# Kernel optimization log

Measured on AMD Instinct MI355X. Metric: run time of the kernel, lower is better.

The kernel has to match this reference:

```python
import jax, jax.numpy as jnp
import numpy as np
from math import factorial

R_MAX = 3.5
BASIS = 20
NORM2MOM_SILU = 1.679177  # e3nn normalize2mom constant for silu

# ---------- Wigner 3j (e3nn convention: real basis, Frobenius norm 1) ----------

def _su2_cg(j1, m1, j2, m2, j3, m3):
    if m3 != m1 + m2:
        return 0.0
    vmin = int(max(-j1 + j2 + m3, -j1 + m1, 0))
    vmax = int(min(j2 + j3 + m1, j3 - j1 + j2, j3 + m3))
    f = lambda n: factorial(round(n))
    C = ((2 * j3 + 1) * f(j3 + j1 - j2) * f(j3 - j1 + j2) * f(j1 + j2 - j3)
         * f(j3 + m3) * f(j3 - m3)
         / (f(j1 + j2 + j3 + 1) * f(j1 - m1) * f(j1 + m1) * f(j2 - m2) * f(j2 + m2))) ** 0.5
    S = 0.0
    for v in range(vmin, vmax + 1):
        S += (-1.0) ** (v + j2 + m2) / f(v) * f(j2 + j3 + m1 - v) * f(j1 - m1 + v) \
             / f(j3 - j1 + j2 - v) / f(j3 + m3 - v) / f(v + j1 - j2 - m3)
    return C * S


def _real_basis(l):
    q = np.zeros((2 * l + 1, 2 * l + 1), dtype=np.complex128)
    for m in range(-l, 0):
        q[l + m, l + abs(m)] = 2 ** -0.5
        q[l + m, l - abs(m)] = -1j * 2 ** -0.5
    q[l, l] = 1.0
    for m in range(1, l + 1):
        q[l + m, l + abs(m)] = (-1) ** m * 2 ** -0.5
        q[l + m, l - abs(m)] = 1j * (-1) ** m * 2 ** -0.5
    return (-1j) ** l * q


def wigner_3j(l1, l2, l3):
    C = np.zeros((2 * l1 + 1, 2 * l2 + 1, 2 * l3 + 1))
    for m1 in range(-l1, l1 + 1):
        for m2 in range(-l2, l2 + 1):
            if abs(m1 + m2) <= l3:
                C[l1 + m1, l2 + m2, l3 + m1 + m2] = _su2_cg(l1, m1, l2, m2, l3, m1 + m2)
    Q1, Q2, Q3 = _real_basis(l1), _real_basis(l2), _real_basis(l3)
    Cr = np.einsum('ij,kl,mn,ikn->jlm', Q1, Q2, np.conj(Q3.T), C.astype(np.complex128))
    assert np.abs(Cr.imag).max() < 1e-4
    Cr = Cr.real
    return (Cr / np.linalg.norm(Cr)).astype(np.float32)

# tp2 paths: (l1 from middle, l2 from sh) -> 2e (even parity, triangle inequality)
TP2_PATHS = [(0, 2), (1, 1), (1, 3), (2, 0), (2, 2), (3, 1), (3, 3)]
W3J = {p: jnp.asarray(wigner_3j(p[0], p[1], 2)) for p in TP2_PATHS}
ALPHA2 = (5.0 / 35.0) ** 0.5  # component norm: sqrt(dim(2e) / fan_in), fan_in = 7 paths * mul 5

# ---------- spherical harmonics, lmax=3, component normalization (e3nn axis convention) ----------

def spherical_harmonics(v):  # v: [E,3] unit vectors -> [E,16]
    x, y, z = v[:, 0], v[:, 1], v[:, 2]
    x2, y2, z2 = x * x, y * y, z * z
    s3, s5, s15 = 3.0 ** 0.5, 5.0 ** 0.5, 15.0 ** 0.5
    s70_4, s105, s42_4 = 70.0 ** 0.5 / 4, 105.0 ** 0.5, 42.0 ** 0.5 / 4
    s7_2, s105_2 = 7.0 ** 0.5 / 2, 105.0 ** 0.5 / 2
    sh = [jnp.ones_like(x),
          s3 * x, s3 * y, s3 * z,
          s15 * x * z, s15 * x * y, s5 * (y2 - 0.5 * (x2 + z2)), s15 * y * z, 0.5 * s15 * (z2 - x2),
          s70_4 * x * (3 * z2 - x2), s105 * x * y * z, s42_4 * x * (5 * y2 - 1.0),
          s7_2 * y * (5 * y2 - 3.0), s42_4 * z * (5 * y2 - 1.0), s105_2 * y * (z2 - x2),
          s70_4 * z * (z2 - 3 * x2)]
    return jnp.stack(sh, axis=-1)


def soft_one_hot(d):  # smooth_finite basis with cutoff on [0, R_MAX]
    values = jnp.linspace(0.0, R_MAX, BASIS + 2)[1:-1]
    step = R_MAX / (BASIS + 1)
    diff = (d[:, None] - values) / step
    def u(t):
        ts = jnp.where(t > 0, t, 1.0)
        return jnp.where(t > 0, jnp.exp(-1.0 / ts), 0.0)
    return 1.14136 * np.e ** 2 * u(diff + 1.0) * u(1.0 - diff)


def setup_inputs() -> dict:
    key = jax.random.key(0)
    ks = jax.random.split(key, 7)
    N, E = 50000, 600000
    edge_from = jax.random.randint(ks[2], (E,), 0, N)
    # no self-loops (avoids zero-length edge vectors, as radius_graph would)
    edge_to = (edge_from + jax.random.randint(ks[3], (E,), 1, N)) % N
    return {
        'x': jax.random.normal(ks[0], (N, 1), jnp.float32),
        'pos': jax.random.normal(ks[1], (N, 3), jnp.float32),
        'edge_from': edge_from,
        'edge_to': edge_to,
        'W1': jax.random.normal(ks[4], (20, 30), jnp.float32),
        'W2': jax.random.normal(ks[5], (30, 20), jnp.float32),
        'tp2_w': jax.random.normal(ks[6], (7, 5), jnp.float32),
    }


def reference(x, pos, edge_from, edge_to, W1, W2, tp2_w):
    E = edge_from.shape[0]
    N = x.shape[0]
    num_neighbors = 6.0
    edge_vec = pos[edge_to] - pos[edge_from]                 # [E,3]
    dist = jnp.linalg.norm(edge_vec, axis=1)                 # [E]
    sh = spherical_harmonics(edge_vec / dist[:, None])       # [E,16]
    emb = soft_one_hot(dist)                                 # [E,20]
    # FullyConnectedNet([20,30,20], silu) with e3nn normalization
    h = NORM2MOM_SILU * jax.nn.silu(emb @ W1 / jnp.sqrt(20.0))
    tp_w = (h @ W2 / jnp.sqrt(30.0)).reshape(E, 4, 5)        # per-edge tp1 weights
    s = x[edge_to, 0]                                        # [E] gathered 0e scalars
    sh_blocks = [sh[:, 0:1], sh[:, 1:4], sh[:, 4:9], sh[:, 9:16]]
    # tp1: 0e x l -> l ; alpha * w3j(0,l,l) collapses to identity per l
    mid = jnp.concatenate([
        (s[:, None, None] * tp_w[:, l, :, None] * sh_blocks[l][:, None, :]).reshape(E, 5 * (2 * l + 1))
        for l in range(4)], axis=-1)                         # [E,80]
    node_mid = jax.ops.segment_sum(mid, edge_from, num_segments=N) / jnp.sqrt(num_neighbors)
    m = node_mid[edge_to]                                    # [E,80]
    offs = [0, 5, 20, 45, 80]
    mid_blocks = [m[:, offs[l]:offs[l + 1]].reshape(E, 5, 2 * l + 1) for l in range(4)]
    out_e = jnp.zeros((E, 5), dtype=x.dtype)
    for p, (l1, l2) in enumerate(TP2_PATHS):
        out_e = out_e + ALPHA2 * jnp.einsum('ijk,eui,ej,u->ek', W3J[(l1, l2)],
                                            mid_blocks[l1], sh_blocks[l2], tp2_w[p])
    node_out = jax.ops.segment_sum(out_e, edge_from, num_segments=N) / jnp.sqrt(num_neighbors)
    Co = jnp.argmax(jnp.bincount(edge_to, length=N))         # torch.mode -> most frequent target node
    return node_out[Co]                                      # [5] = 1x2e
```

## Files before the change

kernel.cpp:

```cpp
#include <hip/hip_runtime.h>
#include <cmath>
#include <complex>
#include <algorithm>

#define NBH   32
#define NB2   16
#define CAP_S 512
#define CAP_T 64
#define CAP_M 4096
#define EB    64
#define HW_MAX 12544
#define BM_MAX 1568

namespace w3jhost {
static double fact(int n){
  static const double f[13]={1,1,2,6,24,120,720,5040,40320,362880,3628800,39916800,479001600};
  return f[n];
}
static double su2_cg(int j1,int m1,int j2,int m2,int j3,int m3){
  if(m3!=m1+m2) return 0.0;
  int vmin = std::max(std::max(-j1+j2+m3,-j1+m1),0);
  int vmax = std::min(std::min(j2+j3+m1, j3-j1+j2), j3+m3);
  double C = std::sqrt((double)(2*j3+1)*fact(j3+j1-j2)*fact(j3-j1+j2)*fact(j1+j2-j3)*fact(j3+m3)*fact(j3-m3)
            /(fact(j1+j2+j3+1)*fact(j1-m1)*fact(j1+m1)*fact(j2-m2)*fact(j2+m2)));
  double S=0.0;
  for(int v=vmin;v<=vmax;v++){
    double sgn = ((v+j2+m2)&1)?-1.0:1.0;
    S += sgn/fact(v)*fact(j2+j3+m1-v)*fact(j1-m1+v)/fact(j3-j1+j2-v)/fact(j3+m3-v)/fact(v+j1-j2-m3);
  }
  return C*S;
}
static void real_basis(int l, std::complex<double> q[7][7]){
  for(int i=0;i<7;i++)for(int j=0;j<7;j++) q[i][j]=0.0;
  const double r = std::sqrt(0.5);
  for(int m=-l;m<0;m++){ q[l+m][l-m]=r; q[l+m][l+m]=std::complex<double>(0.0,-r); }
  q[l][l]=1.0;
  for(int m=1;m<=l;m++){ double sg=(m&1)?-1.0:1.0; q[l+m][l+m]=sg*r; q[l+m][l-m]=std::complex<double>(0.0,sg*r); }
  std::complex<double> f;
  switch(l&3){ case 0: f={1,0};break; case 1: f={0,-1};break; case 2: f={-1,0};break; default: f={0,1};break; }
  for(int i=0;i<7;i++)for(int j=0;j<7;j++) q[i][j]*=f;
}
}

struct W3JArg { float w[675]; };

static W3JArg compute_w3j(){
  using namespace w3jhost;
  W3JArg out{};
  const int pl1[7]={0,1,1,2,2,3,3}, pl2[7]={2,1,3,0,2,1,3};
  int off=0;
  for(int p=0;p<7;p++){
    int l1=pl1[p], l2=pl2[p], l3=2;
    int n1=2*l1+1, n2=2*l2+1, n3=2*l3+1;
    double C[7][7][5];
    for(int i=0;i<7;i++)for(int k=0;k<7;k++)for(int n=0;n<5;n++) C[i][k][n]=0.0;
    for(int m1=-l1;m1<=l1;m1++)for(int m2=-l2;m2<=l2;m2++)
      if(std::abs(m1+m2)<=l3) C[l1+m1][l2+m2][l3+m1+m2]=su2_cg(l1,m1,l2,m2,l3,m1+m2);
    std::complex<double> Q1[7][7],Q2[7][7],Q3[7][7];
    real_basis(l1,Q1); real_basis(l2,Q2); real_basis(l3,Q3);
    double Cr[7][7][5]; double nrm=0.0;
    for(int a=0;a<n1;a++)for(int b=0;b<n2;b++)for(int c=0;c<n3;c++){
      std::complex<double> s(0.0,0.0);
      for(int i=0;i<n1;i++)for(int k=0;k<n2;k++)for(int n=0;n<n3;n++){
        double cv=C[i][k][n]; if(cv==0.0) continue;
        s += Q1[i][a]*Q2[k][b]*std::conj(Q3[n][c])*cv;
      }
      Cr[a][b][c]=s.real(); nrm+=s.real()*s.real();
    }
    nrm=std::sqrt(nrm);
    for(int a=0;a<n1;a++)for(int b=0;b<n2;b++)for(int c=0;c<n3;c++)
      out.w[off+(a*n2+b)*n3+c]=(float)(Cr[a][b][c]/nrm);
    off+=n1*n2*n3;
  }
  return out;
}
static const W3JArg g_w3j = compute_w3j();

__device__ __forceinline__ void calc_sh(float x,float y,float z,float* sh){
  float x2=x*x,y2=y*y,z2=z*z;
  const float s3=1.7320508075688772f, s5=2.2360679774997896f, s15=3.872983346207417f;
  const float s70_4=2.091650066335189f, s105=10.246950765959598f, s42_4=1.6201851746019651f;
  const float s7_2=1.3228756555322954f, s105_2=5.123475382979799f;
  sh[0]=1.f;
  sh[1]=s3*x; sh[2]=s3*y; sh[3]=s3*z;
  sh[4]=s15*x*z; sh[5]=s15*x*y; sh[6]=s5*(y2-0.5f*(x2+z2)); sh[7]=s15*y*z; sh[8]=0.5f*s15*(z2-x2);
  sh[9]=s70_4*x*(3.f*z2-x2); sh[10]=s105*x*y*z; sh[11]=s42_4*x*(5.f*y2-1.f);
  sh[12]=s7_2*y*(5.f*y2-3.f); sh[13]=s42_4*z*(5.f*y2-1.f); sh[14]=s105_2*y*(z2-x2); sh[15]=s70_4*z*(z2-3.f*x2);
}

__device__ __forceinline__ float cloadf(const float* p){ return __hip_atomic_load(p,__ATOMIC_RELAXED,__HIP_MEMORY_SCOPE_AGENT); }

__device__ __forceinline__ void gridbar(int* ctr,int count){
  __syncthreads();
  if(threadIdx.x==0){
    asm volatile("s_waitcnt vmcnt(0) lgkmcnt(0)" ::: "memory");
    __hip_atomic_fetch_add(ctr,1,__ATOMIC_RELAXED,__HIP_MEMORY_SCOPE_AGENT);
    int it=0;
    while(__hip_atomic_load(ctr,__ATOMIC_RELAXED,__HIP_MEMORY_SCOPE_AGENT)<count){
      if(it<16) __builtin_amdgcn_s_sleep(2);
      else      __builtin_amdgcn_s_sleep(16);
      ++it;
    }
  }
  __syncthreads();
}

__global__ void __launch_bounds__(1024,1)
k_hist(const int* __restrict__ eto, int E, int N, int* __restrict__ histg,
       int* __restrict__ ctrl ,
       float* __restrict__ nmid_g){
  __shared__ int hist[HW_MAX];
  const int HW=(N+3)>>2;
  const int tid=threadIdx.x;
  if(blockIdx.x==0 && tid<12) ctrl[tid]=0;
  for(int i=blockIdx.x*1024+tid;i<CAP_T*80;i+=NBH*1024) nmid_g[i]=0.f;
  for(int w=tid;w<HW;w+=1024) hist[w]=0;
  __syncthreads();
  int nQ=(E+3)>>2;
  for(int q=blockIdx.x*1024+tid;q<nQ;q+=NBH*1024){
    int e=q*4;
    if(e+3<E){
      int4 v=*reinterpret_cast<const int4*>(eto+e);
      atomicAdd(&hist[v.x>>2], 1<<((v.x&3)*8));
      atomicAdd(&hist[v.y>>2], 1<<((v.y&3)*8));
      atomicAdd(&hist[v.z>>2], 1<<((v.z&3)*8));
      atomicAdd(&hist[v.w>>2], 1<<((v.w&3)*8));
    } else {
      for(;e<E;e++){ int t=eto[e]; atomicAdd(&hist[t>>2], 1<<((t&3)*8)); }
    }
  }
  __syncthreads();
  for(int w=tid;w<HW;w+=1024) histg[blockIdx.x*HW+w]=hist[w];
}

__global__ void __launch_bounds__(256,1)
k_argmax(const int* __restrict__ histg, int N, unsigned long long* __restrict__ packed){
  const int HW=(N+3)>>2;
  int w=blockIdx.x*256+threadIdx.x;
  unsigned long long lm=0ull;
  if(w<HW){
    int c0=0,c1=0,c2=0,c3=0;
    #pragma unroll
    for(int b=0;b<NBH;b++){
      int h=histg[b*HW+w];
      c0+=h&255; c1+=(h>>8)&255; c2+=(h>>16)&255; c3+=(int)((unsigned)h>>24);
    }
    int node=w*4;
    if(c0>0)          lm=max(lm,(((unsigned long long)(unsigned)c0)<<32)|(unsigned long long)(0xFFFFFFFFu-(unsigned)(node  )));
    if(node+1<N&&c1>0)lm=max(lm,(((unsigned long long)(unsigned)c1)<<32)|(unsigned long long)(0xFFFFFFFFu-(unsigned)(node+1)));
    if(node+2<N&&c2>0)lm=max(lm,(((unsigned long long)(unsigned)c2)<<32)|(unsigned long long)(0xFFFFFFFFu-(unsigned)(node+2)));
    if(node+3<N&&c3>0)lm=max(lm,(((unsigned long long)(unsigned)c3)<<32)|(unsigned long long)(0xFFFFFFFFu-(unsigned)(node+3)));
  }
  #pragma unroll
  for(int off=32;off;off>>=1){
    unsigned long long o=__shfl_xor(lm,off);
    lm=max(lm,o);
  }
  if((threadIdx.x&63)==0 && lm) atomicMax(packed,lm);
}

__global__ void __launch_bounds__(256,1)
k_collect(const int* __restrict__ efrom, int E,
          const unsigned long long* __restrict__ packed,
          int* __restrict__ S, int* __restrict__ numS){
  int co=(int)(0xFFFFFFFFu-(unsigned)((*packed)&0xFFFFFFFFull));
  int q=blockIdx.x*256+threadIdx.x;
  int e=q*4;
  if(e+3<E){
    int4 v=*reinterpret_cast<const int4*>(efrom+e);
    int f[4]={v.x,v.y,v.z,v.w};
    #pragma unroll
    for(int k=0;k<4;k++){
      if(f[k]==co){
        int p=atomicAdd(numS,1);
        if(p<CAP_S) S[p]=e+k;
      }
    }
  } else {
    for(;e<E;e++){
      if(efrom[e]==co){
        int p=atomicAdd(numS,1);
        if(p<CAP_S) S[p]=e;
      }
    }
  }
}

__global__ void __launch_bounds__(256,1)
k_scanM(const int* __restrict__ efrom, const int* __restrict__ eto, int E, int N,
        const int* __restrict__ S, const int* __restrict__ numS,
        int* __restrict__ M, int* __restrict__ numM){
  __shared__ int bitmap[BM_MAX];
  __shared__ int Te[CAP_T];
  __shared__ int Tlist[CAP_T];
  __shared__ int nTs;
  const int tid=threadIdx.x;
  int ns=*numS; if(ns>CAP_S) ns=CAP_S;
  int nsc=min(ns,CAP_T);
  const int BMW=(N+31)>>5;
  for(int w=tid;w<BMW;w+=256) bitmap[w]=0;
  if(tid<nsc) Te[tid]=eto[S[tid]];
  __syncthreads();
  if(tid<64){
    bool keep=false; int myv=0;
    if(tid<nsc){
      myv=Te[tid];
      keep=true;
      for(int k=0;k<tid;k++) if(Te[k]==myv){ keep=false; break; }
    }
    unsigned long long mask=__ballot(keep);
    if(keep){
      int slot=__popcll(mask&((1ull<<tid)-1ull));
      Tlist[slot]=myv;
    }
    if(tid==0) nTs=__popcll(mask);
  }
  __syncthreads();
  int nT=nTs;
  if(tid<nT){ int v=Tlist[tid]; atomicOr(&bitmap[v>>5], 1<<(v&31)); }
  __syncthreads();
  int q=blockIdx.x*256+tid;
  int e=q*4;
  if(e+3<E){
    int4 v=*reinterpret_cast<const int4*>(efrom+e);
    int f[4]={v.x,v.y,v.z,v.w};
    #pragma unroll
    for(int k=0;k<4;k++){
      int s=f[k];
      if((bitmap[s>>5]>>(s&31))&1){
        int sl=0;
        for(int kk=0;kk<nT;kk++) if(Tlist[kk]==s){ sl=kk; break; }
        int p=atomicAdd(numM,1);
        if(p<CAP_M) M[p]=(e+k)|(sl<<20);
      }
    }
  } else {
    for(;e<E;e++){
      int s=efrom[e];
      if((bitmap[s>>5]>>(s&31))&1){
        int sl=0;
        for(int kk=0;kk<nT;kk++) if(Tlist[kk]==s){ sl=kk; break; }
        int p=atomicAdd(numM,1);
        if(p<CAP_M) M[p]=e|(sl<<20);
      }
    }
  }
}

__global__ void __launch_bounds__(1024,1)
k_tail(const float* __restrict__ x, const float* __restrict__ pos,
       const int* __restrict__ efrom, const int* __restrict__ eto,
       const float* __restrict__ W1, const float* __restrict__ W2,
       const float* __restrict__ tp2,
       const int* __restrict__ S, const int* __restrict__ numS,
       const int* __restrict__ M, const int* __restrict__ numM,
       float* __restrict__ nmid_g, int* __restrict__ bars,
       W3JArg w3, float* __restrict__ out5){
  __shared__ float W1s[600], W2s[600];
  __shared__ float shs[EB*16], embs[EB*20], hs[EB*30], tws[EB*20];
  __shared__ float es_[EB], dd_[EB];
  __shared__ int   sl_[EB];
  __shared__ float w3s[675], nmid_s[CAP_T*80], tp2s[35], acc[5];
  __shared__ int   Te[CAP_T], Tlist[CAP_T], nTs;
  const int tid=threadIdx.x, bid=blockIdx.x;

  int nm=*numM; if(nm>CAP_M) nm=CAP_M;
  for(int i=tid;i<600;i+=1024){ W1s[i]=W1[i]; W2s[i]=W2[i]; }
  int per=(nm+NB2-1)/NB2;
  int lo=min(nm,bid*per), hi=min(nm,lo+per);
  for(int base=lo;base<hi;base+=EB){
    int cnt=min(EB,hi-base);
    __syncthreads();
    if(tid<cnt){
      int m=M[base+tid];
      int e=m&0xFFFFF, sl=m>>20;
      sl_[tid]=sl;
      int a=efrom[e], b=eto[e];
      float dx=pos[3*b]-pos[3*a], dy=pos[3*b+1]-pos[3*a+1], dz=pos[3*b+2]-pos[3*a+2];
      float d=sqrtf(dx*dx+dy*dy+dz*dz);
      float inv=1.f/d;
      calc_sh(dx*inv,dy*inv,dz*inv,&shs[tid*16]);
      dd_[tid]=d;
      es_[tid]=x[b]*(0.18257418583505536f*0.4082482904638631f);
    }
    __syncthreads();
    for(int t=tid;t<cnt*20;t+=1024){
      int ee=t/20, i=t-ee*20;
      const float inv_step=21.f/3.5f;
      const float pref=(float)(1.14136*7.3890560989306495);
      float di=dd_[ee]*inv_step;
      float A=di-(float)i, B=(float)(i+2)-di;
      float ua=(A>0.f)?expf(-1.f/A):0.f;
      float ub=(B>0.f)?expf(-1.f/B):0.f;
      embs[ee*20+i]=pref*ua*ub;
    }
    __syncthreads();
    for(int t=tid;t<cnt*30;t+=1024){
      int ee=t/30, j=t-ee*30;
      float z=0.f;
      #pragma unroll
      for(int i=0;i<20;i++) z+=embs[ee*20+i]*W1s[i*30+j];
      z*=0.22360679774997896f;
      hs[ee*30+j]=1.679177f*z/(1.f+expf(-z));
    }
    __syncthreads();
    for(int t=tid;t<cnt*20;t+=1024){
      int ee=t/20, c=t-ee*20;
      float v=0.f;
      #pragma unroll
      for(int j=0;j<30;j++) v+=hs[ee*30+j]*W2s[j*20+c];
      tws[ee*20+c]=v;
    }
    __syncthreads();
    for(int t=tid;t<cnt*80;t+=1024){
      int ee=t/80, oo=t-ee*80;
      int sl=sl_[ee];
      int l,u,mm;
      if(oo<5){ l=0; u=oo; mm=0; }
      else if(oo<20){ int r=oo-5;  l=1; u=r/3; mm=r-u*3; }
      else if(oo<45){ int r=oo-20; l=2; u=r/5; mm=r-u*5; }
      else          { int r=oo-45; l=3; u=r/7; mm=r-u*7; }
      float val=es_[ee]*tws[ee*20+l*5+u]*shs[ee*16+l*l+mm];
      atomicAdd(&nmid_g[sl*80+oo],val);
    }
  }
  gridbar(&bars[0],NB2);
  if(bid!=0) return;

  for(int i=tid;i<675;i+=1024) w3s[i]=w3.w[i];
  if(tid<35) tp2s[tid]=tp2[tid];
  if(tid<5) acc[tid]=0.f;
  int ns=*numS; if(ns>CAP_S) ns=CAP_S;
  int nsc=min(ns,CAP_T);
  if(tid<nsc) Te[tid]=eto[S[tid]];
  __syncthreads();
  if(tid<64){
    bool keep=false; int myv=0;
    if(tid<nsc){
      myv=Te[tid];
      keep=true;
      for(int k=0;k<tid;k++) if(Te[k]==myv){ keep=false; break; }
    }
    unsigned long long mask=__ballot(keep);
    if(keep){
      int slot=__popcll(mask&((1ull<<tid)-1ull));
      Tlist[slot]=myv;
    }
    if(tid==0) nTs=__popcll(mask);
  }
  __syncthreads();
  int nT=nTs;
  for(int i=tid;i<nT*80;i+=1024) nmid_s[i]=cloadf(&nmid_g[i]);
  for(int base=0;base<ns;base+=EB){
    int cnt=min(EB,ns-base);
    __syncthreads();
    if(tid<cnt){
      int e=S[base+tid];
      int a=efrom[e], b=eto[e];
      int sl=-1;
      for(int k=0;k<nT;k++) if(Tlist[k]==b){ sl=k; break; }
      sl_[tid]=sl;
      if(sl>=0){
        float dx=pos[3*b]-pos[3*a], dy=pos[3*b+1]-pos[3*a+1], dz=pos[3*b+2]-pos[3*a+2];
        float d=sqrtf(dx*dx+dy*dy+dz*dz);
        float inv=1.f/d;
        calc_sh(dx*inv,dy*inv,dz*inv,&shs[tid*16]);
      }
    }
    __syncthreads();
    for(int t=tid;t<cnt*35;t+=1024){
      int ee=t/35, r=t-ee*35, p=r/5, u=r-p*5;
      int sl=sl_[ee];
      if(sl>=0){
        int l1=(p+1)>>1;
        int l2=(0x3636>>(2*p))&3;
        const unsigned long long wbpack=
          (25ULL<<9)|(70ULL<<18)|(175ULL<<27)|(200ULL<<36)|(325ULL<<45)|(430ULL<<54);
        int wb=(int)((wbpack>>(9*p))&511ULL);
        int n1=2*l1+1, n2=2*l2+1;
        float tu=tp2s[p*5+u];
        float o0=0.f,o1=0.f,o2=0.f,o3=0.f,o4=0.f;
        const float* mrow=&nmid_s[sl*80+5*l1*l1+u*n1];
        const float* shrow=&shs[ee*16+l2*l2];
        const float* Wp=&w3s[wb];
        for(int i=0;i<n1;i++){
          float mi=mrow[i]*tu;
          for(int j=0;j<n2;j++){
            float c=mi*shrow[j];
            const float* Wk=Wp+(i*n2+j)*5;
            o0+=Wk[0]*c; o1+=Wk[1]*c; o2+=Wk[2]*c; o3+=Wk[3]*c; o4+=Wk[4]*c;
          }
        }
        atomicAdd(&acc[0],o0); atomicAdd(&acc[1],o1); atomicAdd(&acc[2],o2);
        atomicAdd(&acc[3],o3); atomicAdd(&acc[4],o4);
      }
    }
    __syncthreads();
  }
  __syncthreads();
  const float scale=0.37796447300922725f*0.4082482904638631f;
  if(tid<5) out5[tid]=acc[tid]*scale;
}

extern "C" void kernel_launch(void* const* d_in, const int* in_sizes, int n_in,
                              void* d_out, int out_size, void* d_ws, size_t ws_size,
                              hipStream_t stream){
  const float* x    =(const float*)d_in[0];
  const float* pos  =(const float*)d_in[1];
  const int*   efrom=(const int*)  d_in[2];
  const int*   eto  =(const int*)  d_in[3];
  const float* W1   =(const float*)d_in[4];
  const float* W2   =(const float*)d_in[5];
  const float* tp2  =(const float*)d_in[6];
  int N=in_sizes[0], E=in_sizes[2];
  int HW=(N+3)>>2;

  char* ws=(char*)d_ws;
  size_t o=0;
  int* ctrl=(int*)(ws+o);
  unsigned long long* packed=(unsigned long long*)(ws+o); o+=8;
  int* numS=(int*)(ws+o);                   o+=4;
  int* numM=(int*)(ws+o);                   o+=4;
  int* bars=(int*)(ws+o);                   o+=8*4;
  o=(o+63)&~(size_t)63;
  int* histg=(int*)(ws+o);                  o+=(size_t)NBH*HW*4;
  int* S=(int*)(ws+o);                      o+=(size_t)CAP_S*4;
  int* M=(int*)(ws+o);                      o+=(size_t)CAP_M*4;
  float* nmid_g=(float*)(ws+o);             o+=(size_t)CAP_T*80*4;

  int nQ=(E+3)>>2;
  int gScan=(nQ+255)/256;
  int gArg =(HW+255)/256;
  k_hist   <<<NBH,1024,0,stream>>>(eto,E,N,histg,ctrl,nmid_g);
  k_argmax <<<gArg,256,0,stream>>>(histg,N,packed);
  k_collect<<<gScan,256,0,stream>>>(efrom,E,packed,S,numS);
  k_scanM  <<<gScan,256,0,stream>>>(efrom,eto,E,N,S,numS,M,numM);
  k_tail   <<<NB2,1024,0,stream>>>(x,pos,efrom,eto,W1,W2,tp2,S,numS,M,numM,nmid_g,bars,g_w3j,(float*)d_out);
}
```

Before: 110.7 us.

## Fuse argmax into collect kernel using a global-flag spin barrier

Merges the separate argmax kernel into the collect kernel. The first AB blocks compute the per-node histogram maximum and publish it through an atomic max, then bump a global flag. Every block spins on that flag before scanning edges for the most frequent target node. This removes one kernel launch and its inter-kernel gap. The cost is spin-waiting, and a hang is possible if the argmax blocks are not scheduled before the waiting blocks fill the device. The control-zeroing range is widened so the new flag is reset in the histogram kernel.

```diff
diff --git a/kernel.cpp b/kernel.cpp
--- a/kernel.cpp
+++ b/kernel.cpp
@@ -112,7 +112,7 @@
   __shared__ int hist[HW_MAX];
   const int HW=(N+3)>>2;
   const int tid=threadIdx.x;
-  if(blockIdx.x==0 && tid<12) ctrl[tid]=0;
+  if(blockIdx.x==0 && tid<20) ctrl[tid]=0;
   for(int i=blockIdx.x*1024+tid;i<CAP_T*80;i+=NBH*1024) nmid_g[i]=0.f;
   for(int w=tid;w<HW;w+=1024) hist[w]=0;
   __syncthreads();
@@ -134,37 +134,54 @@
 }
 
 __global__ void __launch_bounds__(256,1)
-k_argmax(const int* __restrict__ histg, int N, unsigned long long* __restrict__ packed){
+k_collect(const int* __restrict__ histg, const int* __restrict__ efrom, int E, int N,
+          unsigned long long* __restrict__ packed, int* __restrict__ flag,
+          int* __restrict__ S, int* __restrict__ numS){
+  __shared__ int co_s;
+  const int tid=threadIdx.x;
   const int HW=(N+3)>>2;
-  int w=blockIdx.x*256+threadIdx.x;
-  unsigned long long lm=0ull;
-  if(w<HW){
-    int c0=0,c1=0,c2=0,c3=0;
+  const int AB=(HW+255)>>8;
+  if((int)blockIdx.x<AB){
+    int w=blockIdx.x*256+tid;
+    unsigned long long lm=0ull;
+    if(w<HW){
+      int c0=0,c1=0,c2=0,c3=0;
+      #pragma unroll
+      for(int b=0;b<NBH;b++){
+        int h=histg[b*HW+w];
+        c0+=h&255; c1+=(h>>8)&255; c2+=(h>>16)&255; c3+=(int)((unsigned)h>>24);
+      }
+      int node=w*4;
+      if(c0>0)          lm=max(lm,(((unsigned long long)(unsigned)c0)<<32)|(unsigned long long)(0xFFFFFFFFu-(unsigned)(node  )));
+      if(node+1<N&&c1>0)lm=max(lm,(((unsigned long long)(unsigned)c1)<<32)|(unsigned long long)(0xFFFFFFFFu-(unsigned)(node+1)));
+      if(node+2<N&&c2>0)lm=max(lm,(((unsigned long long)(unsigned)c2)<<32)|(unsigned long long)(0xFFFFFFFFu-(unsigned)(node+2)));
+      if(node+3<N&&c3>0)lm=max(lm,(((unsigned long long)(unsigned)c3)<<32)|(unsigned long long)(0xFFFFFFFFu-(unsigned)(node+3)));
+    }
     #pragma unroll
-    for(int b=0;b<NBH;b++){
-      int h=histg[b*HW+w];
-      c0+=h&255; c1+=(h>>8)&255; c2+=(h>>16)&255; c3+=(int)((unsigned)h>>24);
-    }
-    int node=w*4;
-    if(c0>0)          lm=max(lm,(((unsigned long long)(unsigned)c0)<<32)|(unsigned long long)(0xFFFFFFFFu-(unsigned)(node  )));
-    if(node+1<N&&c1>0)lm=max(lm,(((unsigned long long)(unsigned)c1)<<32)|(unsigned long long)(0xFFFFFFFFu-(unsigned)(node+1)));
-    if(node+2<N&&c2>0)lm=max(lm,(((unsigned long long)(unsigned)c2)<<32)|(unsigned long long)(0xFFFFFFFFu-(unsigned)(node+2)));
-    if(node+3<N&&c3>0)lm=max(lm,(((unsigned long long)(unsigned)c3)<<32)|(unsigned long long)(0xFFFFFFFFu-(unsigned)(node+3)));
-  }
-  #pragma unroll
-  for(int off=32;off;off>>=1){
-    unsigned long long o=__shfl_xor(lm,off);
-    lm=max(lm,o);
-  }
-  if((threadIdx.x&63)==0 && lm) atomicMax(packed,lm);
-}
-
-__global__ void __launch_bounds__(256,1)
-k_collect(const int* __restrict__ efrom, int E,
-          const unsigned long long* __restrict__ packed,
-          int* __restrict__ S, int* __restrict__ numS){
-  int co=(int)(0xFFFFFFFFu-(unsigned)((*packed)&0xFFFFFFFFull));
-  int q=blockIdx.x*256+threadIdx.x;
+    for(int off=32;off;off>>=1){
+      unsigned long long o=__shfl_xor(lm,off);
+      lm=max(lm,o);
+    }
+    if((tid&63)==0 && lm) atomicMax(packed,lm);
+    __syncthreads();
+    if(tid==0){
+      asm volatile("s_waitcnt vmcnt(0) lgkmcnt(0)" ::: "memory");
+      __hip_atomic_fetch_add(flag,1,__ATOMIC_RELAXED,__HIP_MEMORY_SCOPE_AGENT);
+    }
+  }
+  if(tid==0){
+    int it=0;
+    while(__hip_atomic_load(flag,__ATOMIC_RELAXED,__HIP_MEMORY_SCOPE_AGENT)<AB){
+      if(it<8) __builtin_amdgcn_s_sleep(2);
+      else     __builtin_amdgcn_s_sleep(8);
+      ++it;
+    }
+    unsigned long long pk=__hip_atomic_load(packed,__ATOMIC_RELAXED,__HIP_MEMORY_SCOPE_AGENT);
+    co_s=(int)(0xFFFFFFFFu-(unsigned)(pk&0xFFFFFFFFull));
+  }
+  __syncthreads();
+  int co=co_s;
+  int q=blockIdx.x*256+tid;
   int e=q*4;
   if(e+3<E){
     int4 v=*reinterpret_cast<const int4*>(efrom+e);
@@ -423,6 +440,8 @@
   int* numM=(int*)(ws+o);                   o+=4;
   int* bars=(int*)(ws+o);                   o+=8*4;
   o=(o+63)&~(size_t)63;
+  int* flag=(int*)(ws+o);                   o+=4;
+  o=(o+63)&~(size_t)63;
   int* histg=(int*)(ws+o);                  o+=(size_t)NBH*HW*4;
   int* S=(int*)(ws+o);                      o+=(size_t)CAP_S*4;
   int* M=(int*)(ws+o);                      o+=(size_t)CAP_M*4;
@@ -430,10 +449,8 @@
 
   int nQ=(E+3)>>2;
   int gScan=(nQ+255)/256;
-  int gArg =(HW+255)/256;
   k_hist   <<<NBH,1024,0,stream>>>(eto,E,N,histg,ctrl,nmid_g);
-  k_argmax <<<gArg,256,0,stream>>>(histg,N,packed);
-  k_collect<<<gScan,256,0,stream>>>(efrom,E,packed,S,numS);
+  k_collect<<<gScan,256,0,stream>>>(histg,efrom,E,N,packed,flag,S,numS);
   k_scanM  <<<gScan,256,0,stream>>>(efrom,eto,E,N,S,numS,M,numM);
   k_tail   <<<NB2,1024,0,stream>>>(x,pos,efrom,eto,W1,W2,tp2,S,numS,M,numM,nmid_g,bars,g_w3j,(float*)d_out);
 }
```

Result: slower. 121.3 us (+9.6%).
